# Performance work log

Hardware: AMD Instinct MI355X
Metric: run time of the kernel (lower is better)

The kernel has to match this reference:

```python
import jax, jax.numpy as jnp
import numpy as np

BATCH = 4096
NUM_CLASSES = 10000
FEAT_DIM = 512


def setup_inputs() -> dict:
    key = jax.random.key(0)
    k1, k2, k3 = jax.random.split(key, 3)
    x = jax.random.normal(k1, (BATCH, FEAT_DIM), dtype=jnp.float32)
    labels = jax.random.randint(k2, (BATCH,), 0, NUM_CLASSES)
    centers = jax.random.normal(k3, (NUM_CLASSES, FEAT_DIM), dtype=jnp.float32)
    lr = jnp.array([0.1], dtype=jnp.float32)
    return {"x": x, "labels": labels, "centers": centers, "lr": lr}


def reference(x, labels, centers, lr):
    batch, feat_dim = x.shape
    n_classes = centers.shape[0]

    # --- center update (vectorized replacement of the per-class/per-sample double loop) ---
    # A_j = count_j * centers[j] - sum_{i: label_i==j} x_i ;  delta_j = A_j / (1 + count_j)
    ones = jnp.ones((batch,), dtype=x.dtype)
    counts = jax.ops.segment_sum(ones, labels, num_segments=n_classes)          # [C]
    sum_x = jax.ops.segment_sum(x, labels, num_segments=n_classes)              # [C, D]
    delta = (counts[:, None] * centers - sum_x) / (1.0 + counts[:, None])       # [C, D]
    # torch wraps the result in a fresh nn.Parameter -> detached from autograd graph
    centers_new = jax.lax.stop_gradient(centers - lr[0] * delta)

    # --- pairwise squared distances, then 1/(1+d) ---
    d = (jnp.sum(x * x, axis=1, keepdims=True)                                   # [B, 1]
         + jnp.sum(centers_new * centers_new, axis=1)[None, :]                   # [1, C]
         - 2.0 * (x @ centers_new.T))                                            # [B, C]
    d = 1.0 / (1.0 + d)

    # --- masked reduction: row sum minus the own-class entry, clamped ---
    row_sum = d.sum(axis=1)                                                      # [B]
    own = jnp.take_along_axis(d, labels[:, None], axis=1)[:, 0]                  # [B]
    dist = jnp.clip(row_sum - own, 1e-12, 1e12)
    return dist.mean()
```

## Files before the change

### kernel.cpp

```cpp
#include <hip/hip_runtime.h>
#include <hip/hip_bf16.h>

#define BATCH 4096
#define NCLS  10000
#define CPAD  10240
#define FDIM  512
#define MAXL  32

typedef float f32x4 __attribute__((ext_vector_type(4)));
typedef int   ix4   __attribute__((ext_vector_type(4)));
typedef int   ix8   __attribute__((ext_vector_type(8)));

__device__ static inline void gld_lds16(const void* g, void* l) {
    __builtin_amdgcn_global_load_lds(
        (const __attribute__((address_space(1))) void*)g,
        (__attribute__((address_space(3))) void*)l, 16, 0, 0);
}

__device__ static inline unsigned int fp4e(float v) {
    unsigned int s = (__float_as_uint(v) >> 31) << 3;
    float a = fabsf(v);
    unsigned int c;
    if      (a < 1.25f) c = (a < 0.75f) ? (a < 0.25f ? 0u : 1u) : 2u;
    else if (a < 2.5f)  c = (a < 1.75f) ? 3u : 4u;
    else                c = (a < 3.5f) ? 5u : (a < 5.f ? 6u : 7u);
    return s | c;
}

__device__ static inline int pdst4(int row, int k) {
    return (row >> 4) * 4096 + (k >> 7) * 1024
         + ((k >> 5) & 3) * 256 + (row & 15) * 16 + ((k & 31) >> 1);
}

__global__ void prep_all(const float* __restrict__ x, const int* __restrict__ labels,
                         const float* __restrict__ centers, const float* __restrict__ lr,
                         unsigned char* __restrict__ xq, float* __restrict__ xnorm,
                         unsigned char* __restrict__ cq, float* __restrict__ cnorm,
                         float* __restrict__ out) {
    const int bid = blockIdx.x, t = threadIdx.x;
    __shared__ float red[4];
    if (bid < BATCH) {
        if (bid == 0 && t == 0) out[0] = 0.f;
        int i = bid;
        float2 v = *(const float2*)&x[(size_t)i * FDIM + 2 * t];
        xq[pdst4(i, 2 * t)] = (unsigned char)(fp4e(v.x) | (fp4e(v.y) << 4));
        float s = v.x * v.x + v.y * v.y;
#pragma unroll
        for (int m = 1; m < 64; m <<= 1) s += __shfl_xor(s, m);
        if ((t & 63) == 0) red[t >> 6] = s;
        __syncthreads();
        if (t == 0) xnorm[i] = red[0] + red[1] + red[2] + red[3];
        return;
    }
    int j = bid - BATCH;
    if (j >= NCLS) {
        cq[pdst4(j, 2 * t)] = 0;
        if (t == 0) cnorm[j] = 1e30f;
        return;
    }
    __shared__ int nmatch;
    __shared__ int idxs[MAXL];
    if (t == 0) nmatch = 0;
    __syncthreads();
    {
        const int4* l4 = (const int4*)labels;
        int4 a0 = l4[t], a1 = l4[t + 256], a2 = l4[t + 512], a3 = l4[t + 768];
#define CHK(V, B) { \
        if (V.x == j) { int p = atomicAdd(&nmatch, 1); if (p < MAXL) idxs[p] = (B); } \
        if (V.y == j) { int p = atomicAdd(&nmatch, 1); if (p < MAXL) idxs[p] = (B) + 1; } \
        if (V.z == j) { int p = atomicAdd(&nmatch, 1); if (p < MAXL) idxs[p] = (B) + 2; } \
        if (V.w == j) { int p = atomicAdd(&nmatch, 1); if (p < MAXL) idxs[p] = (B) + 3; } }
        CHK(a0, 4 * t) CHK(a1, 4 * (t + 256)) CHK(a2, 4 * (t + 512)) CHK(a3, 4 * (t + 768))
#undef CHK
    }
    __syncthreads();
    int cfull = nmatch;
    int c = cfull > MAXL ? MAXL : cfull;
    if (t == 0 && c > 1) {
        for (int a = 1; a < c; ++a) {
            int v = idxs[a]; int b = a - 1;
            while (b >= 0 && idxs[b] > v) { idxs[b + 1] = idxs[b]; --b; }
            idxs[b + 1] = v;
        }
    }
    __syncthreads();
    float cf  = (float)cfull;
    float lr0 = lr[0];
    float inv = 1.f / (1.f + cf);
    float c0 = centers[(size_t)j * FDIM + 2 * t];
    float c1 = centers[(size_t)j * FDIM + 2 * t + 1];
    float sx0 = 0.f, sx1 = 0.f;
    for (int q = 0; q < c; ++q) {
        const float* xr = &x[(size_t)idxs[q] * FDIM + 2 * t];
        sx0 += xr[0]; sx1 += xr[1];
    }
    float n0 = c0 - lr0 * (cf * c0 - sx0) * inv;
    float n1 = c1 - lr0 * (cf * c1 - sx1) * inv;
    cq[pdst4(j, 2 * t)] = (unsigned char)(fp4e(n0) | (fp4e(n1) << 4));
    float cn2 = n0 * n0 + n1 * n1;
#pragma unroll
    for (int m = 1; m < 64; m <<= 1) cn2 += __shfl_xor(cn2, m);
    if ((t & 63) == 0) red[t >> 6] = cn2;
    __syncthreads();
    if (t == 0) cnorm[j] = red[0] + red[1] + red[2] + red[3];
}

__global__ void __launch_bounds__(256, 4)
pairwise(const unsigned char* __restrict__ xq, const unsigned char* __restrict__ cq,
         const float* __restrict__ xnorm, const float* __restrict__ cnorm,
         const int* __restrict__ labels, float* __restrict__ row_part) {
    __shared__ unsigned char Als[2][8192];
    __shared__ unsigned char Bls[2][8192];
    const int tid = threadIdx.x;
    const int w = tid >> 6, lane = tid & 63;
    const int lr16 = lane & 15, lhi = lane >> 4;
    const int bid = blockIdx.x;
    const int swz = (bid & 7) * 320 + (bid >> 3);
    const int bx = swz & 31, by = swz >> 5;
    const int m_blk = bx * 128, n_blk = by * 128;
    const int mq = (w >> 1) * 64, nq = (w & 1) * 64;

    f32x4 acc[4][4];
#pragma unroll
    for (int a = 0; a < 4; ++a)
#pragma unroll
        for (int b = 0; b < 4; ++b) acc[a][b] = (f32x4)0.f;

    const unsigned char* gA[2];
    const unsigned char* gB[2];
    int ldst[2];
#pragma unroll
    for (int q = 0; q < 2; ++q) {
        gA[q] = xq + (size_t)((m_blk >> 4) + q * 4 + w) * 4096 + lane * 16;
        gB[q] = cq + (size_t)((n_blk >> 4) + q * 4 + w) * 4096 + lane * 16;
        ldst[q] = (q * 4 + w) * 1024 + lane * 16;
    }

#define STAGE(BUF, KT2) { \
    _Pragma("unroll") for (int q = 0; q < 2; ++q) { \
        gld_lds16(gA[q] + (KT2) * 1024, &Als[BUF][ldst[q]]); \
        gld_lds16(gB[q] + (KT2) * 1024, &Bls[BUF][ldst[q]]); } }

#define COMPUTE(BUF) { \
    ix8 af[4], bg[4]; \
    _Pragma("unroll") for (int mi = 0; mi < 4; ++mi) { \
        ix4 lo = *(const ix4*)&Als[BUF][((mq >> 4) + mi) * 1024 + lane * 16]; \
        af[mi] = __builtin_shufflevector(lo, lo, 0, 1, 2, 3, 0, 1, 2, 3); } \
    _Pragma("unroll") for (int ni = 0; ni < 4; ++ni) { \
        ix4 lo = *(const ix4*)&Bls[BUF][((nq >> 4) + ni) * 1024 + lane * 16]; \
        bg[ni] = __builtin_shufflevector(lo, lo, 0, 1, 2, 3, 0, 1, 2, 3); } \
    __builtin_amdgcn_s_setprio(1); \
    _Pragma("unroll") for (int mi = 0; mi < 4; ++mi) \
    _Pragma("unroll") for (int ni = 0; ni < 4; ++ni) \
        acc[mi][ni] = __builtin_amdgcn_mfma_scale_f32_16x16x128_f8f6f4( \
            bg[ni], af[mi], acc[mi][ni], 4, 4, 0, 0x7F7F7F7F, 0, 0x7F7F7F7F); \
    __builtin_amdgcn_s_setprio(0); }

    STAGE(0, 0)
#pragma unroll
    for (int t = 0; t < 3; ++t) {
        if ((t & 1) == 0) { STAGE(1, t + 1) }
        else              { STAGE(0, t + 1) }
        asm volatile("s_waitcnt vmcnt(4)" ::: "memory");
        __builtin_amdgcn_s_barrier();
        if ((t & 1) == 0) { COMPUTE(0) }
        else              { COMPUTE(1) }
        __builtin_amdgcn_sched_barrier(0);
        __builtin_amdgcn_s_barrier();
    }
    asm volatile("s_waitcnt vmcnt(0)" ::: "memory");
    __builtin_amdgcn_s_barrier();
    COMPUTE(1)

    float rsum[4];
#pragma unroll
    for (int mi = 0; mi < 4; ++mi) {
        int m_g = m_blk + mq + mi * 16 + lr16;
        float xn1 = 1.f + xnorm[m_g];
        int lab = labels[m_g];
        float s = 0.f;
#pragma unroll
        for (int ni = 0; ni < 4; ++ni) {
#pragma unroll
            for (int r = 0; r < 4; ++r) {
                int n_g = n_blk + nq + ni * 16 + lhi * 4 + r;
                float d1 = xn1 + cnorm[n_g] - 2.f * acc[mi][ni][r];
                float rc = __builtin_amdgcn_rcpf(d1);
                s += (n_g != lab) ? rc : 0.f;
            }
        }
        s += __shfl_xor(s, 16);
        s += __shfl_xor(s, 32);
        rsum[mi] = s;
    }
    float* spart = (float*)&Als[0][0];
    if ((w & 1) && lhi == 0) {
#pragma unroll
        for (int mi = 0; mi < 4; ++mi)
            spart[mq + mi * 16 + lr16] = rsum[mi];
    }
    __syncthreads();
    if (!(w & 1) && lhi == 0) {
        float* rp = row_part + (size_t)by * BATCH + m_blk;
#pragma unroll
        for (int mi = 0; mi < 4; ++mi) {
            int ml = mq + mi * 16 + lr16;
            rp[ml] = rsum[mi] + spart[ml];
        }
    }
#undef STAGE
#undef COMPUTE
}

__global__ void finalize(const float* __restrict__ row_part, float* __restrict__ out) {
    int i = blockIdx.x * 256 + threadIdx.x;
    float s = 0.f;
    for (int p = 0; p < CPAD / 128; ++p) s += row_part[(size_t)p * BATCH + i];
    float dist = fminf(fmaxf(s, 1e-12f), 1e12f);
    float v = dist * (1.f / BATCH);
#pragma unroll
    for (int m = 1; m < 64; m <<= 1) v += __shfl_xor(v, m);
    __shared__ float red[4];
    if ((threadIdx.x & 63) == 0) red[threadIdx.x >> 6] = v;
    __syncthreads();
    if (threadIdx.x == 0) atomicAdd(out, red[0] + red[1] + red[2] + red[3]);
}

extern "C" void kernel_launch(void* const* d_in, const int* in_sizes, int n_in,
                              void* d_out, int out_size, void* d_ws, size_t ws_size,
                              hipStream_t stream) {
    const float* x       = (const float*)d_in[0];
    const int*   labels  = (const int*)d_in[1];
    const float* centers = (const float*)d_in[2];
    const float* lr      = (const float*)d_in[3];
    float* out = (float*)d_out;

    char* ws = (char*)d_ws;
    size_t off = 0;
    unsigned char* cq = (unsigned char*)(ws + off); off += (size_t)CPAD * FDIM / 2;
    unsigned char* xq = (unsigned char*)(ws + off); off += (size_t)BATCH * FDIM / 2;
    float* cnorm    = (float*)(ws + off); off += (size_t)CPAD * 4;
    float* xnorm    = (float*)(ws + off); off += (size_t)BATCH * 4;
    float* row_part = (float*)(ws + off); off += (size_t)(CPAD / 128) * BATCH * 4;

    prep_all<<<BATCH + CPAD, 256, 0, stream>>>(x, labels, centers, lr,
                                               xq, xnorm, cq, cnorm, out);
    pairwise<<<(BATCH / 128) * (CPAD / 128), 256, 0, stream>>>(xq, cq, xnorm, cnorm, labels, row_part);
    finalize<<<BATCH / 256, 256, 0, stream>>>(row_part, out);
}
```

Measured before the change: 45.14 us.

## Load full K tile into LDS at once instead of double-buffered pipeline

The pairwise GEMM kernel drops its double-buffered staging loop. It now issues every global-to-LDS load for the whole K extent (64KB of fp4 tiles) up front, waits once, and then runs four MFMA steps with no intermediate barriers. This removes the per-step barriers and waitcnt synchronisation. In exchange, LDS use per block grows from 32KB to 64KB, so occupancy is lowered (launch bounds go from 4 to 2 blocks per CU), and load latency is no longer overlapped with compute inside a block. A barrier is added before the LDS is reused for the row-sum partials.

```diff
diff --git a/kernel.cpp b/kernel.cpp
--- a/kernel.cpp
+++ b/kernel.cpp
@@ -105,12 +105,12 @@
     if (t == 0) cnorm[j] = red[0] + red[1] + red[2] + red[3];
 }
 
-__global__ void __launch_bounds__(256, 4)
+__global__ void __launch_bounds__(256, 2)
 pairwise(const unsigned char* __restrict__ xq, const unsigned char* __restrict__ cq,
          const float* __restrict__ xnorm, const float* __restrict__ cnorm,
          const int* __restrict__ labels, float* __restrict__ row_part) {
-    __shared__ unsigned char Als[2][8192];
-    __shared__ unsigned char Bls[2][8192];
+    __shared__ unsigned char Als[32768];
+    __shared__ unsigned char Bls[32768];
     const int tid = threadIdx.x;
     const int w = tid >> 6, lane = tid & 63;
     const int lr16 = lane & 15, lhi = lane >> 4;
@@ -126,51 +126,38 @@
 #pragma unroll
         for (int b = 0; b < 4; ++b) acc[a][b] = (f32x4)0.f;
 
-    const unsigned char* gA[2];
-    const unsigned char* gB[2];
-    int ldst[2];
-#pragma unroll
-    for (int q = 0; q < 2; ++q) {
-        gA[q] = xq + (size_t)((m_blk >> 4) + q * 4 + w) * 4096 + lane * 16;
-        gB[q] = cq + (size_t)((n_blk >> 4) + q * 4 + w) * 4096 + lane * 16;
-        ldst[q] = (q * 4 + w) * 1024 + lane * 16;
-    }
-
-#define STAGE(BUF, KT2) { \
-    _Pragma("unroll") for (int q = 0; q < 2; ++q) { \
-        gld_lds16(gA[q] + (KT2) * 1024, &Als[BUF][ldst[q]]); \
-        gld_lds16(gB[q] + (KT2) * 1024, &Bls[BUF][ldst[q]]); } }
-
-#define COMPUTE(BUF) { \
-    ix8 af[4], bg[4]; \
-    _Pragma("unroll") for (int mi = 0; mi < 4; ++mi) { \
-        ix4 lo = *(const ix4*)&Als[BUF][((mq >> 4) + mi) * 1024 + lane * 16]; \
-        af[mi] = __builtin_shufflevector(lo, lo, 0, 1, 2, 3, 0, 1, 2, 3); } \
-    _Pragma("unroll") for (int ni = 0; ni < 4; ++ni) { \
-        ix4 lo = *(const ix4*)&Bls[BUF][((nq >> 4) + ni) * 1024 + lane * 16]; \
-        bg[ni] = __builtin_shufflevector(lo, lo, 0, 1, 2, 3, 0, 1, 2, 3); } \
-    __builtin_amdgcn_s_setprio(1); \
-    _Pragma("unroll") for (int mi = 0; mi < 4; ++mi) \
-    _Pragma("unroll") for (int ni = 0; ni < 4; ++ni) \
-        acc[mi][ni] = __builtin_amdgcn_mfma_scale_f32_16x16x128_f8f6f4( \
-            bg[ni], af[mi], acc[mi][ni], 4, 4, 0, 0x7F7F7F7F, 0, 0x7F7F7F7F); \
-    __builtin_amdgcn_s_setprio(0); }
-
-    STAGE(0, 0)
-#pragma unroll
-    for (int t = 0; t < 3; ++t) {
-        if ((t & 1) == 0) { STAGE(1, t + 1) }
-        else              { STAGE(0, t + 1) }
-        asm volatile("s_waitcnt vmcnt(4)" ::: "memory");
-        __builtin_amdgcn_s_barrier();
-        if ((t & 1) == 0) { COMPUTE(0) }
-        else              { COMPUTE(1) }
-        __builtin_amdgcn_sched_barrier(0);
-        __builtin_amdgcn_s_barrier();
+    const unsigned char* gA = xq + (size_t)(m_blk >> 4) * 4096 + tid * 16;
+    const unsigned char* gB = cq + (size_t)(n_blk >> 4) * 4096 + tid * 16;
+#pragma unroll
+    for (int q = 0; q < 8; ++q) {
+        gld_lds16(gA + q * 4096, &Als[q * 4096 + tid * 16]);
+        gld_lds16(gB + q * 4096, &Bls[q * 4096 + tid * 16]);
     }
     asm volatile("s_waitcnt vmcnt(0)" ::: "memory");
     __builtin_amdgcn_s_barrier();
-    COMPUTE(1)
+
+#pragma unroll
+    for (int kt2 = 0; kt2 < 4; ++kt2) {
+        ix8 af[4], bg[4];
+#pragma unroll
+        for (int mi = 0; mi < 4; ++mi) {
+            ix4 lo = *(const ix4*)&Als[((mq >> 4) + mi) * 4096 + kt2 * 1024 + lane * 16];
+            af[mi] = __builtin_shufflevector(lo, lo, 0, 1, 2, 3, 0, 1, 2, 3);
+        }
+#pragma unroll
+        for (int ni = 0; ni < 4; ++ni) {
+            ix4 lo = *(const ix4*)&Bls[((nq >> 4) + ni) * 4096 + kt2 * 1024 + lane * 16];
+            bg[ni] = __builtin_shufflevector(lo, lo, 0, 1, 2, 3, 0, 1, 2, 3);
+        }
+        __builtin_amdgcn_s_setprio(1);
+#pragma unroll
+        for (int mi = 0; mi < 4; ++mi)
+#pragma unroll
+            for (int ni = 0; ni < 4; ++ni)
+                acc[mi][ni] = __builtin_amdgcn_mfma_scale_f32_16x16x128_f8f6f4(
+                    bg[ni], af[mi], acc[mi][ni], 4, 4, 0, 0x7F7F7F7F, 0, 0x7F7F7F7F);
+        __builtin_amdgcn_s_setprio(0);
+    }
 
     float rsum[4];
 #pragma unroll
@@ -193,7 +180,8 @@
         s += __shfl_xor(s, 32);
         rsum[mi] = s;
     }
-    float* spart = (float*)&Als[0][0];
+    __syncthreads();
+    float* spart = (float*)&Als[0];
     if ((w & 1) && lhi == 0) {
 #pragma unroll
         for (int mi = 0; mi < 4; ++mi)
@@ -208,8 +196,6 @@
             rp[ml] = rsum[mi] + spart[ml];
         }
     }
-#undef STAGE
-#undef COMPUTE
 }
 
 __global__ void finalize(const float* __restrict__ row_part, float* __restrict__ out) {
```

New measurement: 47.44 us. 5.1% more time.
